# Performance work log

Measured on AMD Instinct MI355X. Metric: run time of the kernel, lower is better.

The kernel has to match this reference:

```python
import jax, jax.numpy as jnp
import numpy as np

NUM_HEADS = 16

def setup_inputs() -> dict:
    key = jax.random.key(0)
    k1, k2, k3 = jax.random.split(key, 3)
    B, N, C = 2, 2048, 1024
    x = jax.random.normal(k1, (B, N, C), dtype=jnp.float32)
    w_qkv = jax.random.normal(k2, (C, 3 * C), dtype=jnp.float32) * (C ** -0.5)
    w_proj = jax.random.normal(k3, (C, C), dtype=jnp.float32) * (C ** -0.5)
    b_proj = jnp.zeros((C,), dtype=jnp.float32)
    return {"x": x, "w_qkv": w_qkv, "w_proj": w_proj, "b_proj": b_proj}

def reference(x, w_qkv, w_proj, b_proj):
    B, N, C = x.shape
    H = NUM_HEADS
    D = C // H
    scale = D ** -0.5
    qkv = x @ w_qkv                               # [B,N,3C]
    qkv = qkv.reshape(B, N, 3, H, D).transpose(2, 0, 3, 1, 4)  # [3,B,H,N,D]
    q, k, v = qkv[0] * scale, qkv[1], qkv[2]
    attn = jnp.einsum('bhnd,bhmd->bhnm', q, k)    # [B,H,N,N]
    attn = jax.nn.softmax(attn, axis=-1)
    out = jnp.einsum('bhnm,bhmd->bhnd', attn, v)  # [B,H,N,D]
    out = out.transpose(0, 2, 1, 3).reshape(B, N, C)
    return out @ w_proj + b_proj
```

## Files before the change

kernel.cpp:

```cpp
#include <hip/hip_runtime.h>

typedef unsigned short ushort_t;
typedef __attribute__((ext_vector_type(8))) short short8;
typedef __attribute__((ext_vector_type(4))) float f32x4;

#define AS1 __attribute__((address_space(1)))
#define AS3 __attribute__((address_space(3)))

#define EXP2F(x) __builtin_amdgcn_exp2f(x)

__device__ __forceinline__ ushort_t f2bf(float f) {
    union { float f; unsigned u; } v; v.f = f;
    unsigned r = v.u + 0x7fffu + ((v.u >> 16) & 1u);
    return (ushort_t)(r >> 16);
}

__device__ __forceinline__ unsigned pack_bf16_pair(float a, float b) {
    unsigned ua = __float_as_uint(a) + 0x8000u;
    unsigned ub = __float_as_uint(b) + 0x8000u;
    return __builtin_amdgcn_perm(ub, ua, 0x07060302u);
}

__device__ __forceinline__ void gl_lds16(const ushort_t* g, ushort_t* lds_base) {
    __builtin_amdgcn_global_load_lds((const AS1 unsigned int*)(size_t)g,
                                     (AS3 unsigned int*)lds_base, 16, 0, 0);
}

#define QSCALE 0.18033688011112042f

__device__ __forceinline__ void transpose_body(
    const float* __restrict__ in, ushort_t* __restrict__ out,
    int K0, int N0, int n, int k0)
{
    ushort_t vals[32];
#pragma unroll
    for (int kk = 0; kk < 32; kk++)
        vals[kk] = f2bf(in[(size_t)(k0 + kk) * N0 + n]);
#pragma unroll
    for (int c = 0; c < 4; c++) {
        short8 v;
#pragma unroll
        for (int e = 0; e < 8; e++) v[e] = (short)vals[c * 8 + e];
        *(short8*)&out[(size_t)n * K0 + k0 + c * 8] = v;
    }
}

__global__ __launch_bounds__(256) void prep_kernel(
    const float* __restrict__ x, const float* __restrict__ wqkv,
    const float* __restrict__ wproj,
    ushort_t* __restrict__ Xb, ushort_t* __restrict__ WqkvT,
    ushort_t* __restrict__ WpT)
{
    const int blk = blockIdx.x, t = threadIdx.x;
    if (blk < 2048) {
        int idx = (blk * 256 + t) * 8;
        float4 a = *(const float4*)&x[idx];
        float4 b = *(const float4*)&x[idx + 4];
        short8 v;
        v[0] = (short)f2bf(a.x); v[1] = (short)f2bf(a.y);
        v[2] = (short)f2bf(a.z); v[3] = (short)f2bf(a.w);
        v[4] = (short)f2bf(b.x); v[5] = (short)f2bf(b.y);
        v[6] = (short)f2bf(b.z); v[7] = (short)f2bf(b.w);
        *(short8*)&Xb[idx] = v;
    } else if (blk < 2048 + 384) {
        int i = blk - 2048;
        transpose_body(wqkv, WqkvT, 1024, 3072, (i % 12) * 256 + t, (i / 12) * 32);
    } else {
        int i = blk - 2432;
        transpose_body(wproj, WpT, 1024, 1024, (i % 4) * 256 + t, (i / 4) * 32);
    }
}

template<int JT>
__device__ __forceinline__ void mfma_gemm_core(
    const ushort_t* __restrict__ A, const ushort_t* __restrict__ Bt,
    int bm, int bn, int w, int lane,
    ushort_t* Atile, ushort_t* Btile, f32x4 acc[4][JT])
{
    const int K = 1024;
    const int wy = w >> 1, wx = w & 1;
    const int lrow8 = lane >> 3;
    const int srcoct = (lane & 7) ^ (lrow8 & 7);
    const int fr = lane & 15, fo = lane >> 4;

    for (int k0 = 0; k0 < K; k0 += 64) {
        __syncthreads();
#pragma unroll
        for (int it = 0; it < 4; it++) {
            int L = w * 4 + it;
            int r = 8 * L + lrow8;
            gl_lds16(A + (size_t)(bm + r) * K + k0 + srcoct * 8, Atile + L * 512);
        }
#pragma unroll
        for (int it = 0; it < JT; it++) {
            int L = w * JT + it;
            int r = 8 * L + lrow8;
            gl_lds16(Bt + (size_t)(bn + r) * K + k0 + srcoct * 8, Btile + L * 512);
        }
        __syncthreads();
#pragma unroll
        for (int s = 0; s < 2; s++) {
            short8 af[4], bf[JT];
#pragma unroll
            for (int i = 0; i < 4; i++) {
                int m = wy * 64 + i * 16 + fr;
                af[i] = *(const short8*)&Atile[m * 64 + (((s * 4 + fo) ^ (m & 7)) * 8)];
            }
#pragma unroll
            for (int j = 0; j < JT; j++) {
                int n = wx * (JT * 16) + j * 16 + fr;
                bf[j] = *(const short8*)&Btile[n * 64 + (((s * 4 + fo) ^ (n & 7)) * 8)];
            }
#pragma unroll
            for (int i = 0; i < 4; i++)
#pragma unroll
                for (int j = 0; j < JT; j++)
                    acc[i][j] = __builtin_amdgcn_mfma_f32_16x16x32_bf16(
                        af[i], bf[j], acc[i][j], 0, 0, 0);
        }
    }
}

__global__ __launch_bounds__(256) void qkv_gemm_kernel(
    const ushort_t* __restrict__ Xb, const ushort_t* __restrict__ WqkvT,
    ushort_t* __restrict__ Qb, ushort_t* __restrict__ Kb, ushort_t* __restrict__ Vtb)
{
    __shared__ __align__(16) ushort_t Atile[128 * 64];
    __shared__ __align__(16) ushort_t Btile[128 * 64];
    const int t = threadIdx.x, w = t >> 6, lane = t & 63;
    const int bm = blockIdx.y * 128, bn = blockIdx.x * 128;

    f32x4 acc[4][4];
#pragma unroll
    for (int i = 0; i < 4; i++)
#pragma unroll
        for (int j = 0; j < 4; j++) acc[i][j] = (f32x4){0.f, 0.f, 0.f, 0.f};

    mfma_gemm_core<4>(Xb, WqkvT, bm, bn, w, lane, Atile, Btile, acc);

    const int wy = w >> 1, wx = w & 1;
    const int colbase = bn + wx * 64 + (lane & 15);
    const int rowbase = bm + wy * 64 + (lane >> 4) * 4;
#pragma unroll
    for (int i = 0; i < 4; i++) {
        int n0 = rowbase + i * 16;
        int b = n0 >> 11, n = n0 & 2047;
#pragma unroll
        for (int j = 0; j < 4; j++) {
            int col = colbase + j * 16;
            f32x4 a = acc[i][j];
            if (col < 1024) {
                int h = col >> 6, d = col & 63;
                size_t base = ((size_t)(b * 16 + h) * 2048 + n) * 64 + d;
#pragma unroll
                for (int r = 0; r < 4; r++)
                    Qb[base + (size_t)r * 64] = f2bf(a[r] * QSCALE);
            } else if (col < 2048) {
                int hc = col & 1023;
                int h = hc >> 6, d = hc & 63;
                size_t base = ((size_t)(b * 16 + h) * 2048 + n) * 64 + d;
#pragma unroll
                for (int r = 0; r < 4; r++)
                    Kb[base + (size_t)r * 64] = f2bf(a[r]);
            } else {
                int hc = col & 1023;
                int h = hc >> 6, d = hc & 63;
                unsigned d0 = pack_bf16_pair(a[0], a[1]);
                unsigned d1 = pack_bf16_pair(a[2], a[3]);
                *(uint2*)&Vtb[((size_t)(b * 16 + h) * 64 + d) * 2048 + n] =
                    make_uint2(d0, d1);
            }
        }
    }
}

__global__ __launch_bounds__(256, 2) void attn_kernel(
    const ushort_t* __restrict__ Q, const ushort_t* __restrict__ K,
    const ushort_t* __restrict__ Vt, ushort_t* __restrict__ O)
{
    __shared__ __align__(16) ushort_t Pbuf[2][128 * 64];
    __shared__ __align__(16) ushort_t Kbuf[2][64 * 64];
    __shared__ __align__(16) ushort_t Vbuf[3][64 * 64];
    __shared__ float l_lds[128];

    const int lin = blockIdx.x;
    const int xcd = lin & 7, slot = lin >> 3;
    const int bh = xcd * 4 + (slot >> 4);
    const int q0 = (slot & 15) * 128;

    const int t = threadIdx.x, w = t >> 6, lane = t & 63;
    const int lrow8 = lane >> 3;
    const int srcoct = (lane & 7) ^ (lrow8 & 7);
    const int fr = lane & 15, fo = lane >> 4;

    const ushort_t* Qh = Q  + (size_t)bh * 2048 * 64;
    const ushort_t* Kh = K  + (size_t)bh * 2048 * 64;
    const ushort_t* Vh = Vt + (size_t)bh * 64 * 2048;

#pragma unroll
    for (int it = 0; it < 4; it++) {
        int L = w * 4 + it;
        int r = 8 * L + lrow8;
        gl_lds16(Qh + (size_t)(q0 + r) * 64 + srcoct * 8, &Pbuf[1][L * 512]);
    }
#pragma unroll
    for (int it = 0; it < 2; it++) {
        int L = w * 2 + it;
        int r = 16 * w + 8 * it + lrow8;
        gl_lds16(Kh + (size_t)r * 64 + srcoct * 8,   &Kbuf[0][L * 512]);
        gl_lds16(Vh + (size_t)r * 2048 + srcoct * 8, &Vbuf[0][L * 512]);
    }
    if (t < 128) l_lds[t] = 0.f;
    __syncthreads();

    short8 qf[8][2];
#pragma unroll
    for (int jq = 0; jq < 8; jq++)
#pragma unroll
        for (int s = 0; s < 2; s++) {
            int m = jq * 16 + fr;
            qf[jq][s] = *(const short8*)&Pbuf[1][m * 64 + (((s * 4 + fo) ^ (m & 7)) * 8)];
        }

    f32x4 o_acc[2][4];
    float l_part[8];
#pragma unroll
    for (int a = 0; a < 2; a++)
#pragma unroll
        for (int jd = 0; jd < 4; jd++) o_acc[a][jd] = (f32x4){0.f, 0.f, 0.f, 0.f};
#pragma unroll
    for (int j = 0; j < 8; j++) l_part[j] = 0.f;

    ushort_t* Vr  = Vbuf[0];
    ushort_t* Vs1 = Vbuf[1];
    ushort_t* Vs2 = Vbuf[2];
    ushort_t* Kr  = Kbuf[0];
    ushort_t* Kn  = Kbuf[1];
    ushort_t* Pa  = Pbuf[0];
    ushort_t* Pb  = Pbuf[1];

    for (int kt = 0; kt < 32; kt++) {
        const int u = (kt + 1) & 31;
#pragma unroll
        for (int it = 0; it < 2; it++) {
            int L = w * 2 + it;
            int r = 16 * w + 8 * it + lrow8;
            gl_lds16(Kh + ((size_t)u * 64 + r) * 64 + srcoct * 8, Kn  + L * 512);
            gl_lds16(Vh + (size_t)r * 2048 + u * 64 + srcoct * 8, Vs1 + L * 512);
        }

        f32x4 s_acc[8];
#pragma unroll
        for (int j = 0; j < 8; j++) s_acc[j] = (f32x4){0.f, 0.f, 0.f, 0.f};
#pragma unroll
        for (int s = 0; s < 2; s++) {
            int mk = 16 * w + fr;
            short8 kf = *(const short8*)&Kr[mk * 64 + (((s * 4 + fo) ^ (mk & 7)) * 8)];
#pragma unroll
            for (int jq = 0; jq < 8; jq++)
                s_acc[jq] = __builtin_amdgcn_mfma_f32_16x16x32_bf16(
                    kf, qf[jq][s], s_acc[jq], 0, 0, 0);
        }

#pragma unroll
        for (int jq = 0; jq < 8; jq++) {
            float p0 = EXP2F(s_acc[jq][0]);
            float p1 = EXP2F(s_acc[jq][1]);
            float p2 = EXP2F(s_acc[jq][2]);
            float p3 = EXP2F(s_acc[jq][3]);
            l_part[jq] += (p0 + p1) + (p2 + p3);
            unsigned d0 = pack_bf16_pair(p0, p1);
            unsigned d1 = pack_bf16_pair(p2, p3);
            int q   = jq * 16 + fr;
            int oct = 2 * w + (fo >> 1);
            int addr = q * 64 + ((oct ^ (q & 7)) * 8) + (fo & 1) * 4;
            *(uint2*)&Pa[addr] = make_uint2(d0, d1);
        }
        __syncthreads();

#pragma unroll
        for (int s = 0; s < 2; s++) {
            short8 pf[2];
#pragma unroll
            for (int a = 0; a < 2; a++) {
                int mq = 32 * w + 16 * a + fr;
                pf[a] = *(const short8*)&Pa[mq * 64 + (((s * 4 + fo) ^ (mq & 7)) * 8)];
            }
#pragma unroll
            for (int jd = 0; jd < 4; jd++) {
                int nd = jd * 16 + fr;
                short8 vf = *(const short8*)&Vr[nd * 64 + (((s * 4 + fo) ^ (nd & 7)) * 8)];
#pragma unroll
                for (int a = 0; a < 2; a++)
                    o_acc[a][jd] = __builtin_amdgcn_mfma_f32_16x16x32_bf16(
                        pf[a], vf, o_acc[a][jd], 0, 0, 0);
            }
        }

        ushort_t* tv = Vr; Vr = Vs1; Vs1 = Vs2; Vs2 = tv;
        ushort_t* tk = Kr; Kr = Kn; Kn = tk;
        ushort_t* tp = Pa; Pa = Pb; Pb = tp;
    }

#pragma unroll
    for (int jq = 0; jq < 8; jq++)
        atomicAdd(&l_lds[jq * 16 + fr], l_part[jq]);
    __syncthreads();

    const int b = bh >> 4, h = bh & 15;
#pragma unroll
    for (int a = 0; a < 2; a++)
#pragma unroll
        for (int r = 0; r < 4; r++) {
            int qrow = 32 * w + 16 * a + fo * 4 + r;
            float inv = 1.f / l_lds[qrow];
            int row = b * 2048 + q0 + qrow;
#pragma unroll
            for (int jd = 0; jd < 4; jd++) {
                int col = h * 64 + jd * 16 + fr;
                O[(size_t)row * 1024 + col] = f2bf(o_acc[a][jd][r] * inv);
            }
        }
}

__global__ __launch_bounds__(256) void proj_gemm_kernel(
    const ushort_t* __restrict__ Ao, const ushort_t* __restrict__ WpT,
    const float* __restrict__ bias, float* __restrict__ out)
{
    __shared__ __align__(16) ushort_t Atile[128 * 64];
    __shared__ __align__(16) ushort_t Btile[64 * 64];
    const int t = threadIdx.x, w = t >> 6, lane = t & 63;
    const int bm = blockIdx.y * 128, bn = blockIdx.x * 64;

    f32x4 acc[4][2];
#pragma unroll
    for (int i = 0; i < 4; i++)
#pragma unroll
        for (int j = 0; j < 2; j++) acc[i][j] = (f32x4){0.f, 0.f, 0.f, 0.f};

    mfma_gemm_core<2>(Ao, WpT, bm, bn, w, lane, Atile, Btile, acc);

    const int wy = w >> 1, wx = w & 1;
    const int colbase = bn + wx * 32 + (lane & 15);
    const int rowbase = bm + wy * 64 + (lane >> 4) * 4;
#pragma unroll
    for (int i = 0; i < 4; i++) {
#pragma unroll
        for (int r = 0; r < 4; r++) {
            int row = rowbase + i * 16 + r;
#pragma unroll
            for (int j = 0; j < 2; j++) {
                int col = colbase + j * 16;
                out[(size_t)row * 1024 + col] = acc[i][j][r] + bias[col];
            }
        }
    }
}

extern "C" void kernel_launch(void* const* d_in, const int* in_sizes, int n_in,
                              void* d_out, int out_size, void* d_ws, size_t ws_size,
                              hipStream_t stream) {
    const float* x      = (const float*)d_in[0];
    const float* w_qkv  = (const float*)d_in[1];
    const float* w_proj = (const float*)d_in[2];
    const float* b_proj = (const float*)d_in[3];
    float* out = (float*)d_out;

    char* ws = (char*)d_ws;
    ushort_t* Xb    = (ushort_t*)(ws);
    ushort_t* WqkvT = (ushort_t*)(ws + ((size_t)8  << 20));
    ushort_t* WpT   = (ushort_t*)(ws + ((size_t)14 << 20));
    ushort_t* Qb    = (ushort_t*)(ws + ((size_t)16 << 20));
    ushort_t* Kb    = (ushort_t*)(ws + ((size_t)24 << 20));
    ushort_t* Vtb   = (ushort_t*)(ws + ((size_t)32 << 20));
    ushort_t* Aob   = (ushort_t*)(ws + ((size_t)40 << 20));

    prep_kernel<<<2560, 256, 0, stream>>>(x, w_qkv, w_proj, Xb, WqkvT, WpT);
    qkv_gemm_kernel<<<dim3(24, 32), 256, 0, stream>>>(Xb, WqkvT, Qb, Kb, Vtb);
    attn_kernel<<<dim3(512), 256, 0, stream>>>(Qb, Kb, Vtb, Aob);
    proj_gemm_kernel<<<dim3(16, 32), 256, 0, stream>>>(Aob, WpT, b_proj, out);
}
```

Baseline: 199.2 us.

## Split attention block across 8 waves and load K fragments directly to registers

The attention kernel moves from 4 to 8 waves per block. Each wave now computes S for a 64-query by 16-key slice and PV for a 32x32 output tile. K fragments are read straight from global memory into registers instead of being staged in LDS, and V/P buffering drops from triple to double buffering, which shrinks LDS use so more blocks fit per CU. This aims to raise occupancy and latency hiding. The cost is exposed global-load latency on the K fragments, since each is read just before the next iteration's score MFMAs, and only one barrier per iteration guards the double-buffered V and P.

New measurement: 203.3 us. 1.02x slower.

```diff
diff --git a/kernel.cpp b/kernel.cpp
--- a/kernel.cpp
+++ b/kernel.cpp
@@ -174,13 +174,12 @@
     }
 }
 
-__global__ __launch_bounds__(256, 2) void attn_kernel(
+__global__ __launch_bounds__(512, 4) void attn_kernel(
     const ushort_t* __restrict__ Q, const ushort_t* __restrict__ K,
     const ushort_t* __restrict__ Vt, ushort_t* __restrict__ O)
 {
     __shared__ __align__(16) ushort_t Pbuf[2][128 * 64];
-    __shared__ __align__(16) ushort_t Kbuf[2][64 * 64];
-    __shared__ __align__(16) ushort_t Vbuf[3][64 * 64];
+    __shared__ __align__(16) ushort_t Vbuf[2][64 * 64];
     __shared__ float l_lds[128];
 
     const int lin = blockIdx.x;
@@ -192,103 +191,102 @@
     const int lrow8 = lane >> 3;
     const int srcoct = (lane & 7) ^ (lrow8 & 7);
     const int fr = lane & 15, fo = lane >> 4;
+    const int kq = w >> 2, kk = w & 3;
+    const int pq = w & 3,  pd = w >> 2;
 
     const ushort_t* Qh = Q  + (size_t)bh * 2048 * 64;
     const ushort_t* Kh = K  + (size_t)bh * 2048 * 64;
     const ushort_t* Vh = Vt + (size_t)bh * 64 * 2048;
 
 #pragma unroll
-    for (int it = 0; it < 4; it++) {
-        int L = w * 4 + it;
+    for (int it = 0; it < 2; it++) {
+        int L = w * 2 + it;
         int r = 8 * L + lrow8;
         gl_lds16(Qh + (size_t)(q0 + r) * 64 + srcoct * 8, &Pbuf[1][L * 512]);
     }
-#pragma unroll
-    for (int it = 0; it < 2; it++) {
-        int L = w * 2 + it;
-        int r = 16 * w + 8 * it + lrow8;
-        gl_lds16(Kh + (size_t)r * 64 + srcoct * 8,   &Kbuf[0][L * 512]);
-        gl_lds16(Vh + (size_t)r * 2048 + srcoct * 8, &Vbuf[0][L * 512]);
-    }
+    {
+        int r = 8 * w + lrow8;
+        gl_lds16(Vh + (size_t)r * 2048 + srcoct * 8, &Vbuf[0][w * 512]);
+    }
+    short8 kf[2];
+#pragma unroll
+    for (int s = 0; s < 2; s++)
+        kf[s] = *(const short8*)&Kh[(size_t)(16 * kk + fr) * 64 + (s * 4 + fo) * 8];
     if (t < 128) l_lds[t] = 0.f;
     __syncthreads();
 
-    short8 qf[8][2];
-#pragma unroll
-    for (int jq = 0; jq < 8; jq++)
+    short8 qf[4][2];
+#pragma unroll
+    for (int jq = 0; jq < 4; jq++)
 #pragma unroll
         for (int s = 0; s < 2; s++) {
-            int m = jq * 16 + fr;
+            int m = 64 * kq + jq * 16 + fr;
             qf[jq][s] = *(const short8*)&Pbuf[1][m * 64 + (((s * 4 + fo) ^ (m & 7)) * 8)];
         }
 
-    f32x4 o_acc[2][4];
-    float l_part[8];
+    f32x4 o_acc[2][2];
+    float l_part[4];
 #pragma unroll
     for (int a = 0; a < 2; a++)
 #pragma unroll
-        for (int jd = 0; jd < 4; jd++) o_acc[a][jd] = (f32x4){0.f, 0.f, 0.f, 0.f};
-#pragma unroll
-    for (int j = 0; j < 8; j++) l_part[j] = 0.f;
-
-    ushort_t* Vr  = Vbuf[0];
-    ushort_t* Vs1 = Vbuf[1];
-    ushort_t* Vs2 = Vbuf[2];
-    ushort_t* Kr  = Kbuf[0];
-    ushort_t* Kn  = Kbuf[1];
-    ushort_t* Pa  = Pbuf[0];
-    ushort_t* Pb  = Pbuf[1];
+        for (int jd = 0; jd < 2; jd++) o_acc[a][jd] = (f32x4){0.f, 0.f, 0.f, 0.f};
+#pragma unroll
+    for (int j = 0; j < 4; j++) l_part[j] = 0.f;
 
     for (int kt = 0; kt < 32; kt++) {
+        ushort_t* Pa = Pbuf[kt & 1];
+        const ushort_t* Vr = Vbuf[kt & 1];
+
+#pragma unroll
+        for (int half = 0; half < 2; half++) {
+            f32x4 s_acc[2];
+            s_acc[0] = (f32x4){0.f, 0.f, 0.f, 0.f};
+            s_acc[1] = (f32x4){0.f, 0.f, 0.f, 0.f};
+#pragma unroll
+            for (int s = 0; s < 2; s++)
+#pragma unroll
+                for (int j = 0; j < 2; j++)
+                    s_acc[j] = __builtin_amdgcn_mfma_f32_16x16x32_bf16(
+                        kf[s], qf[half * 2 + j][s], s_acc[j], 0, 0, 0);
+#pragma unroll
+            for (int j = 0; j < 2; j++) {
+                int jq = half * 2 + j;
+                float p0 = EXP2F(s_acc[j][0]);
+                float p1 = EXP2F(s_acc[j][1]);
+                float p2 = EXP2F(s_acc[j][2]);
+                float p3 = EXP2F(s_acc[j][3]);
+                l_part[jq] += (p0 + p1) + (p2 + p3);
+                unsigned d0 = pack_bf16_pair(p0, p1);
+                unsigned d1 = pack_bf16_pair(p2, p3);
+                int q   = 64 * kq + jq * 16 + fr;
+                int oct = 2 * kk + (fo >> 1);
+                int addr = q * 64 + ((oct ^ (q & 7)) * 8) + (fo & 1) * 4;
+                *(uint2*)&Pa[addr] = make_uint2(d0, d1);
+            }
+        }
+        __syncthreads();
+
         const int u = (kt + 1) & 31;
 #pragma unroll
-        for (int it = 0; it < 2; it++) {
-            int L = w * 2 + it;
-            int r = 16 * w + 8 * it + lrow8;
-            gl_lds16(Kh + ((size_t)u * 64 + r) * 64 + srcoct * 8, Kn  + L * 512);
-            gl_lds16(Vh + (size_t)r * 2048 + u * 64 + srcoct * 8, Vs1 + L * 512);
-        }
-
-        f32x4 s_acc[8];
-#pragma unroll
-        for (int j = 0; j < 8; j++) s_acc[j] = (f32x4){0.f, 0.f, 0.f, 0.f};
-#pragma unroll
-        for (int s = 0; s < 2; s++) {
-            int mk = 16 * w + fr;
-            short8 kf = *(const short8*)&Kr[mk * 64 + (((s * 4 + fo) ^ (mk & 7)) * 8)];
-#pragma unroll
-            for (int jq = 0; jq < 8; jq++)
-                s_acc[jq] = __builtin_amdgcn_mfma_f32_16x16x32_bf16(
-                    kf, qf[jq][s], s_acc[jq], 0, 0, 0);
-        }
-
-#pragma unroll
-        for (int jq = 0; jq < 8; jq++) {
-            float p0 = EXP2F(s_acc[jq][0]);
-            float p1 = EXP2F(s_acc[jq][1]);
-            float p2 = EXP2F(s_acc[jq][2]);
-            float p3 = EXP2F(s_acc[jq][3]);
-            l_part[jq] += (p0 + p1) + (p2 + p3);
-            unsigned d0 = pack_bf16_pair(p0, p1);
-            unsigned d1 = pack_bf16_pair(p2, p3);
-            int q   = jq * 16 + fr;
-            int oct = 2 * w + (fo >> 1);
-            int addr = q * 64 + ((oct ^ (q & 7)) * 8) + (fo & 1) * 4;
-            *(uint2*)&Pa[addr] = make_uint2(d0, d1);
-        }
-        __syncthreads();
+        for (int s = 0; s < 2; s++)
+            kf[s] = *(const short8*)&Kh[(size_t)(u * 64 + 16 * kk + fr) * 64 + (s * 4 + fo) * 8];
+        {
+            int r = 8 * w + lrow8;
+            gl_lds16(Vh + (size_t)r * 2048 + u * 64 + srcoct * 8,
+                     &Vbuf[(kt + 1) & 1][w * 512]);
+        }
 
 #pragma unroll
         for (int s = 0; s < 2; s++) {
             short8 pf[2];
 #pragma unroll
             for (int a = 0; a < 2; a++) {
-                int mq = 32 * w + 16 * a + fr;
+                int mq = 32 * pq + 16 * a + fr;
                 pf[a] = *(const short8*)&Pa[mq * 64 + (((s * 4 + fo) ^ (mq & 7)) * 8)];
             }
 #pragma unroll
-            for (int jd = 0; jd < 4; jd++) {
-                int nd = jd * 16 + fr;
+            for (int jd = 0; jd < 2; jd++) {
+                int nd = 32 * pd + 16 * jd + fr;
                 short8 vf = *(const short8*)&Vr[nd * 64 + (((s * 4 + fo) ^ (nd & 7)) * 8)];
 #pragma unroll
                 for (int a = 0; a < 2; a++)
@@ -296,15 +294,11 @@
                         pf[a], vf, o_acc[a][jd], 0, 0, 0);
             }
         }
-
-        ushort_t* tv = Vr; Vr = Vs1; Vs1 = Vs2; Vs2 = tv;
-        ushort_t* tk = Kr; Kr = Kn; Kn = tk;
-        ushort_t* tp = Pa; Pa = Pb; Pb = tp;
-    }
-
-#pragma unroll
-    for (int jq = 0; jq < 8; jq++)
-        atomicAdd(&l_lds[jq * 16 + fr], l_part[jq]);
+    }
+
+#pragma unroll
+    for (int jq = 0; jq < 4; jq++)
+        atomicAdd(&l_lds[64 * kq + jq * 16 + fr], l_part[jq]);
     __syncthreads();
 
     const int b = bh >> 4, h = bh & 15;
@@ -312,12 +306,12 @@
     for (int a = 0; a < 2; a++)
 #pragma unroll
         for (int r = 0; r < 4; r++) {
-            int qrow = 32 * w + 16 * a + fo * 4 + r;
+            int qrow = 32 * pq + 16 * a + fo * 4 + r;
             float inv = 1.f / l_lds[qrow];
             int row = b * 2048 + q0 + qrow;
 #pragma unroll
-            for (int jd = 0; jd < 4; jd++) {
-                int col = h * 64 + jd * 16 + fr;
+            for (int jd = 0; jd < 2; jd++) {
+                int col = h * 64 + 32 * pd + jd * 16 + fr;
                 O[(size_t)row * 1024 + col] = f2bf(o_acc[a][jd][r] * inv);
             }
         }
@@ -377,6 +371,6 @@
 
     prep_kernel<<<2560, 256, 0, stream>>>(x, w_qkv, w_proj, Xb, WqkvT, WpT);
     qkv_gemm_kernel<<<dim3(24, 32), 256, 0, stream>>>(Xb, WqkvT, Qb, Kb, Vtb);
-    attn_kernel<<<dim3(512), 256, 0, stream>>>(Qb, Kb, Vtb, Aob);
+    attn_kernel<<<dim3(512), 512, 0, stream>>>(Qb, Kb, Vtb, Aob);
     proj_gemm_kernel<<<dim3(16, 32), 256, 0, stream>>>(Aob, WpT, b_proj, out);
 }
```
